# Kernel optimization log

Measured on AMD Instinct MI355X. Metric: run time of the kernel, lower is better.

## Reference

```python
import jax, jax.numpy as jnp
import numpy as np
from jax import lax

N = 50000        # num nodes
E = 800000       # edges per relation (no self loops; N self loops appended)
R = 3            # num_relations
F_IN = 256       # feature_size
C = 128          # hid_dim / channels
B = 4096         # batch_nodes
DT = 0.25
NSTEPS = 4       # n = ceil(time/dt) = ceil(1.0/0.25)


def setup_inputs() -> dict:
    key = jax.random.key(0)
    k1, k2, k3, k4, k5, k6, k7, k8 = jax.random.split(key, 8)
    features = jax.random.normal(k1, (N, F_IN), dtype=jnp.float32)
    # edges with no self loops: dst = (src + off) mod N, off in [1, N)
    src = jax.random.randint(k2, (R, E), 0, N)
    off = jax.random.randint(k3, (R, E), 1, N)
    dst = (src + off) % N
    edge_index = jnp.stack([src, dst], axis=1).astype(jnp.int64)  # [R, 2, E]
    batch_nodes = jax.random.randint(k4, (B,), 0, N).astype(jnp.int64)
    s = 1.0 / np.sqrt(F_IN)
    lin0_w = jax.random.normal(k5, (R, C, F_IN), dtype=jnp.float32) * s
    lin0_b = jax.random.normal(k6, (R, C), dtype=jnp.float32) * 0.01
    lin1_w = jax.random.normal(k7, (R, C, F_IN), dtype=jnp.float32) * s
    lin1_b = jax.random.normal(k8, (R, C), dtype=jnp.float32) * 0.01
    return {"features": features, "edge_index": edge_index, "batch_nodes": batch_nodes,
            "lin0_w": lin0_w, "lin0_b": lin0_b, "lin1_w": lin1_w, "lin1_b": lin1_b}


def _propagate(x, row, col, w):
    # out[i] = sum_{e: col[e]==i} w[e] * x[row[e]]   (gather-scale-scatter SpMM)
    return jax.ops.segment_sum(w[:, None] * x[row], col, num_segments=N)


def _wave_pde(x, row, col, w0, b0, w1, b1):
    # add_remaining_self_loops(fill=0.0): self loops appended at end with weight 0
    loops = jnp.arange(N, dtype=row.dtype)
    row_f = jnp.concatenate([row, loops])
    col_f = jnp.concatenate([col, loops])
    w_f = jnp.concatenate([jnp.ones((E,), x.dtype), jnp.zeros((N,), x.dtype)])
    # sym normalization: D^-1/2 A D^-1/2 (deg over col)
    deg = jax.ops.segment_sum(w_f, col_f, num_segments=N)
    dinv = jnp.where(deg > 0, lax.rsqrt(jnp.maximum(deg, 1e-30)), 0.0)
    w_norm = dinv[row_f] * w_f * dinv[col_f]
    # set_init_value
    phi0 = x @ w0.T + b0
    phi1 = x @ w1.T + b1
    # exp_conv_0 (exp_init=True): w' = dt^2*w/2; diag += 1; x1 = dt*phi1 + prop(phi0)
    w_init = (DT * DT * 0.5) * w_norm
    w_init = w_init.at[E:].add(1.0)
    x1 = DT * phi1 + _propagate(phi0, row_f, col_f, w_init)
    # time-stepping convs: w'' = dt^2*w; diag += 2; x_next = prop(x) - x_pre
    w_step = (DT * DT) * w_norm
    w_step = w_step.at[E:].add(2.0)

    def step(carry, _):
        xc, xp = carry
        xn = _propagate(xc, row_f, col_f, w_step) - xp
        return (xn, xc), None

    (x_out, _), _ = lax.scan(step, (x1, phi0), None, length=NSTEPS - 1)
    return x_out


def reference(features, edge_index, batch_nodes, lin0_w, lin0_b, lin1_w, lin1_b):
    # eval mode: dropout is identity
    embeds = []
    for r in range(R):
        row = edge_index[r, 0]
        col = edge_index[r, 1]
        x = _wave_pde(features, row, col, lin0_w[r], lin0_b[r], lin1_w[r], lin1_b[r])
        embeds.append(x[batch_nodes])  # [B, C]
    multi = jnp.stack(embeds, axis=1)  # [B, R, C]
    return multi.reshape(B, R * C)
```

## Files before the change

kernel.cpp:

```cpp
#include <hip/hip_runtime.h>
#include <hip/hip_bf16.h>

#define N_NODES 50000
#define N_EDGES 800000
#define N_REL   3
#define F_IN    256
#define CH      128
#define BATCH   4096
#define DT      0.25f
#define NRANGE  8
#define RSPAN   6250

typedef __bf16 bf16x8 __attribute__((ext_vector_type(8)));
typedef float f32x4 __attribute__((ext_vector_type(4)));

__device__ __forceinline__ ushort f2bf(float f) {
  unsigned u = __float_as_uint(f);
  return (ushort)((u + 0x7FFFu + ((u >> 16) & 1u)) >> 16);
}
__device__ __forceinline__ float bf2f(ushort h) {
  return __uint_as_float((unsigned)h << 16);
}

__global__ void k_detect(const int* __restrict__ ei, int* __restrict__ flag) {
  int lane = threadIdx.x;
  int v = ei[2 * lane + 1];
  unsigned long long m = __ballot(v != 0);
  if (lane == 0) flag[0] = (m == 0ull) ? 1 : 0;
}

__global__ void k_hist3x(const int* __restrict__ ei, const int* __restrict__ flag,
                         int* __restrict__ deg3) {
  int b = blockIdx.x;
  int q = b & (NRANGE - 1), chunk = b >> 3;
  int e = chunk * 256 + threadIdx.x;
  int r = blockIdx.y;
  if (e >= N_EDGES) return;
  long ci = (long)r * 2 * N_EDGES + N_EDGES + e;
  int d = flag[0] ? ei[2 * ci] : ei[ci];
  if (d / RSPAN == q) atomicAdd(&deg3[r * N_NODES + d], 1);
}

__global__ void k_dinv3(const int* __restrict__ deg3, float* __restrict__ dinv3,
                        int* __restrict__ flag) {
  int i = blockIdx.x * blockDim.x + threadIdx.x;
  if (i >= 3 * N_NODES) return;
  int d = deg3[i];
  if (d > 0) {
    dinv3[i] = rsqrtf((float)d);
  } else {
    dinv3[i] = 0.0f;
    atomicOr(&flag[1], 1);
  }
}

__global__ void k_scan3(const int* __restrict__ deg3, int* __restrict__ off3) {
  __shared__ int sm[1024];
  const int* deg = deg3 + blockIdx.x * N_NODES;
  int* off = off3 + blockIdx.x * (N_NODES + 1);
  int tid = threadIdx.x;
  const int PER = (N_NODES + 1023) / 1024;
  int base = tid * PER;
  int s = 0;
  for (int i = 0; i < PER; ++i) { int idx = base + i; if (idx < N_NODES) s += deg[idx]; }
  sm[tid] = s;
  __syncthreads();
  for (int d = 1; d < 1024; d <<= 1) {
    int v = 0;
    if (tid >= d) v = sm[tid - d];
    __syncthreads();
    sm[tid] += v;
    __syncthreads();
  }
  int run = sm[tid] - s;
  for (int i = 0; i < PER; ++i) {
    int idx = base + i;
    if (idx < N_NODES) { off[idx] = run; run += deg[idx]; }
  }
  if (tid == 1023) off[N_NODES] = run;
}

__global__ void k_fill3x(const int* __restrict__ ei, const int* __restrict__ flag,
                         const int* __restrict__ off3, int* __restrict__ cur3,
                         const float* __restrict__ dinv3, void* __restrict__ csrv) {
  int b = blockIdx.x;
  int q = b & (NRANGE - 1), chunk = b >> 3;
  int e = chunk * 256 + threadIdx.x;
  int r = blockIdx.y;
  if (e >= N_EDGES) return;
  int i64 = flag[0], iso = flag[1];
  long ri = (long)r * 2 * N_EDGES + e;
  long ci = ri + N_EDGES;
  int d = i64 ? ei[2 * ci] : ei[ci];
  if (d / RSPAN != q) return;
  int s = i64 ? ei[2 * ri] : ei[ri];
  int pos = atomicAdd(&cur3[r * N_NODES + d], 1);
  int slot = off3[r * (N_NODES + 1) + d] + pos;
  if (iso) {
    const float* dinv = dinv3 + r * N_NODES;
    ((int2*)csrv)[(size_t)r * N_EDGES + slot] =
        make_int2(s, __float_as_int(dinv[s] * dinv[d]));
  } else {
    ((int*)csrv)[(size_t)r * N_EDGES + slot] = s;
  }
}

__global__ __launch_bounds__(256) void k_phi_mfma(
    const float* __restrict__ X, const float* __restrict__ W0,
    const float* __restrict__ b0, const float* __restrict__ W1,
    const float* __restrict__ b1, const float* __restrict__ dinv,
    const int* __restrict__ flag, float* __restrict__ P0,
    float* __restrict__ P1) {
  __shared__ ushort Ah[128 * 32], Al[128 * 32], Bh[128 * 32], Bl[128 * 32];
  const int tid = threadIdx.x;
  const int m0 = blockIdx.x * 128;
  const float* W = blockIdx.y ? W1 : W0;
  const float* bias = blockIdx.y ? b1 : b0;
  float* P = blockIdx.y ? P1 : P0;
  const int wid = tid >> 6, lane = tid & 63;
  const int wr = wid >> 1, wc = wid & 1;
  const int lr = lane & 15, k8 = lane >> 4;
  const int rt = tid >> 1, kb = (tid & 1) * 16;
  const bool mok = (m0 + rt) < N_NODES;
  const float* Xrow = X + (size_t)(m0 + rt) * F_IN;
  const float* Wrow = W + (size_t)rt * F_IN;
  f32x4 acc[4][4] = {};
  for (int k0 = 0; k0 < F_IN; k0 += 32) {
    float4 xa[4], wb[4];
#pragma unroll
    for (int j = 0; j < 4; ++j) {
      xa[j] = mok ? *(const float4*)(Xrow + k0 + kb + 4 * j)
                  : make_float4(0.f, 0.f, 0.f, 0.f);
      wb[j] = *(const float4*)(Wrow + k0 + kb + 4 * j);
    }
    if (k0) __syncthreads();
#pragma unroll
    for (int j = 0; j < 4; ++j) {
      int idx = rt * 32 + kb + 4 * j;
      ushort h0 = f2bf(xa[j].x), h1 = f2bf(xa[j].y), h2 = f2bf(xa[j].z), h3 = f2bf(xa[j].w);
      *(ushort4*)&Ah[idx] = make_ushort4(h0, h1, h2, h3);
      *(ushort4*)&Al[idx] =
          make_ushort4(f2bf(xa[j].x - bf2f(h0)), f2bf(xa[j].y - bf2f(h1)),
                       f2bf(xa[j].z - bf2f(h2)), f2bf(xa[j].w - bf2f(h3)));
      ushort g0 = f2bf(wb[j].x), g1 = f2bf(wb[j].y), g2 = f2bf(wb[j].z), g3 = f2bf(wb[j].w);
      *(ushort4*)&Bh[idx] = make_ushort4(g0, g1, g2, g3);
      *(ushort4*)&Bl[idx] =
          make_ushort4(f2bf(wb[j].x - bf2f(g0)), f2bf(wb[j].y - bf2f(g1)),
                       f2bf(wb[j].z - bf2f(g2)), f2bf(wb[j].w - bf2f(g3)));
    }
    __syncthreads();
    bf16x8 ah[4], al[4], bh[4], bl[4];
#pragma unroll
    for (int i = 0; i < 4; ++i) {
      int ao = (wr * 64 + i * 16 + lr) * 32 + k8 * 8;
      int bo = (wc * 64 + i * 16 + lr) * 32 + k8 * 8;
      ah[i] = *(const bf16x8*)&Ah[ao];
      al[i] = *(const bf16x8*)&Al[ao];
      bh[i] = *(const bf16x8*)&Bh[bo];
      bl[i] = *(const bf16x8*)&Bl[bo];
    }
#pragma unroll
    for (int i = 0; i < 4; ++i)
#pragma unroll
      for (int j = 0; j < 4; ++j) {
        acc[i][j] = __builtin_amdgcn_mfma_f32_16x16x32_bf16(ah[i], bh[j], acc[i][j], 0, 0, 0);
        acc[i][j] = __builtin_amdgcn_mfma_f32_16x16x32_bf16(ah[i], bl[j], acc[i][j], 0, 0, 0);
        acc[i][j] = __builtin_amdgcn_mfma_f32_16x16x32_bf16(al[i], bh[j], acc[i][j], 0, 0, 0);
      }
  }
  int iso = flag[1];
  float rsc[4][4];
#pragma unroll
  for (int i = 0; i < 4; ++i)
#pragma unroll
    for (int q = 0; q < 4; ++q) {
      int m = m0 + wr * 64 + i * 16 + k8 * 4 + q;
      rsc[i][q] = (m < N_NODES && !iso) ? dinv[m] : 1.0f;
    }
#pragma unroll
  for (int j = 0; j < 4; ++j) {
    int ch = wc * 64 + j * 16 + lr;
    float bv = bias[ch];
#pragma unroll
    for (int i = 0; i < 4; ++i) {
      int mbase = m0 + wr * 64 + i * 16 + k8 * 4;
#pragma unroll
      for (int q = 0; q < 4; ++q) {
        int m = mbase + q;
        if (m < N_NODES) P[(size_t)m * CH + ch] = (acc[i][j][q] + bv) * rsc[i][q];
      }
    }
  }
}

__device__ __forceinline__ void prop_accum(
    const float* __restrict__ xc, const void* __restrict__ csrv, int r, int iso,
    int e0, int e1, int g, int l, float4& acc0, float4& acc1) {
  if (!iso) {
    const int* csr = (const int*)csrv + (size_t)r * N_EDGES;
    for (int e = e0; e < e1; e += 16) {
      int lim = e1 - 1;
      int src[4]; float wgt[4];
#pragma unroll
      for (int u = 0; u < 4; ++u) {
        int ee = e + 4 * u + g;
        src[u] = csr[min(ee, lim)];
        wgt[u] = (ee <= lim) ? 1.f : 0.f;
      }
      float4 va[4], vb[4];
#pragma unroll
      for (int u = 0; u < 4; ++u) {
        const float4* rs = (const float4*)(xc + (size_t)src[u] * CH);
        va[u] = rs[l];
        vb[u] = rs[l + 16];
      }
#pragma unroll
      for (int u = 0; u < 4; ++u) {
        float w0 = wgt[u];
        acc0.x = fmaf(w0, va[u].x, acc0.x); acc0.y = fmaf(w0, va[u].y, acc0.y);
        acc0.z = fmaf(w0, va[u].z, acc0.z); acc0.w = fmaf(w0, va[u].w, acc0.w);
        acc1.x = fmaf(w0, vb[u].x, acc1.x); acc1.y = fmaf(w0, vb[u].y, acc1.y);
        acc1.z = fmaf(w0, vb[u].z, acc1.z); acc1.w = fmaf(w0, vb[u].w, acc1.w);
      }
    }
  } else {
    const int2* csr = (const int2*)csrv + (size_t)r * N_EDGES;
    for (int e = e0; e < e1; e += 16) {
      int lim = e1 - 1;
      int2 pm[4]; float wgt[4];
#pragma unroll
      for (int u = 0; u < 4; ++u) {
        int ee = e + 4 * u + g;
        pm[u] = csr[min(ee, lim)];
        wgt[u] = (ee <= lim) ? __int_as_float(pm[u].y) : 0.f;
      }
      float4 va[4], vb[4];
#pragma unroll
      for (int u = 0; u < 4; ++u) {
        const float4* rs = (const float4*)(xc + (size_t)pm[u].x * CH);
        va[u] = rs[l];
        vb[u] = rs[l + 16];
      }
#pragma unroll
      for (int u = 0; u < 4; ++u) {
        float w0 = wgt[u];
        acc0.x = fmaf(w0, va[u].x, acc0.x); acc0.y = fmaf(w0, va[u].y, acc0.y);
        acc0.z = fmaf(w0, va[u].z, acc0.z); acc0.w = fmaf(w0, va[u].w, acc0.w);
        acc1.x = fmaf(w0, vb[u].x, acc1.x); acc1.y = fmaf(w0, vb[u].y, acc1.y);
        acc1.z = fmaf(w0, vb[u].z, acc1.z); acc1.w = fmaf(w0, vb[u].w, acc1.w);
      }
    }
  }
}

__global__ __launch_bounds__(256, 6) void k_prop(
    const float* __restrict__ xcb, const float* __restrict__ otherb,
    float* __restrict__ outb, const int* __restrict__ off3,
    const void* __restrict__ csrv, const int* __restrict__ flag, int rel0,
    size_t slab, float wscale, float aself, float beta) {
  int node = blockIdx.x * 4 + (threadIdx.x >> 6);
  if (node >= N_NODES) return;
  int rel = rel0 + blockIdx.y;
  const float* xc = xcb + (size_t)blockIdx.y * slab;
  const float* other = otherb + (size_t)blockIdx.y * slab;
  float* out = outb + (size_t)blockIdx.y * slab;
  const int* off = off3 + rel * (N_NODES + 1);
  int iso = flag[1];
  int lane = threadIdx.x & 63;
  int g = lane >> 4, l = lane & 15;
  int e0 = off[node], e1 = off[node + 1];
  size_t base = (size_t)node * CH;
  int go = (g & 1) * 64;
  float4 sv = *(const float4*)(xc + base + go + 4 * l);
  float4 ov = *(const float4*)(other + base + go + 4 * l);
  float4 acc0 = make_float4(0.f, 0.f, 0.f, 0.f);
  float4 acc1 = make_float4(0.f, 0.f, 0.f, 0.f);
  prop_accum(xc, csrv, rel, iso, e0, e1, g, l, acc0, acc1);
#pragma unroll
  for (int m = 16; m < 64; m <<= 1) {
    acc0.x += __shfl_xor(acc0.x, m); acc0.y += __shfl_xor(acc0.y, m);
    acc0.z += __shfl_xor(acc0.z, m); acc0.w += __shfl_xor(acc0.w, m);
    acc1.x += __shfl_xor(acc1.x, m); acc1.y += __shfl_xor(acc1.y, m);
    acc1.z += __shfl_xor(acc1.z, m); acc1.w += __shfl_xor(acc1.w, m);
  }
  float ws2 = iso ? wscale : ((e1 > e0) ? wscale / (float)(e1 - e0) : 0.f);
  if (g == 0) {
    float4 o;
    o.x = ws2 * acc0.x + aself * sv.x + beta * ov.x;
    o.y = ws2 * acc0.y + aself * sv.y + beta * ov.y;
    o.z = ws2 * acc0.z + aself * sv.z + beta * ov.z;
    o.w = ws2 * acc0.w + aself * sv.w + beta * ov.w;
    *(float4*)(out + base + 4 * l) = o;
  } else if (g == 1) {
    float4 o;
    o.x = ws2 * acc1.x + aself * sv.x + beta * ov.x;
    o.y = ws2 * acc1.y + aself * sv.y + beta * ov.y;
    o.z = ws2 * acc1.z + aself * sv.z + beta * ov.z;
    o.w = ws2 * acc1.w + aself * sv.w + beta * ov.w;
    *(float4*)(out + base + 64 + 4 * l) = o;
  }
}

__global__ __launch_bounds__(256) void k_gprop(
    const float* __restrict__ y3b, const float* __restrict__ y2b,
    const int* __restrict__ off3, const void* __restrict__ csrv,
    const int* __restrict__ flag, const int* __restrict__ batch,
    float* __restrict__ out, int rel0, size_t slab,
    float wscale, float aself, float beta) {
  int b = blockIdx.x * 4 + (threadIdx.x >> 6);
  if (b >= BATCH) return;
  int rel = rel0 + blockIdx.y;
  const float* y3 = y3b + (size_t)blockIdx.y * slab;
  const float* y2 = y2b + (size_t)blockIdx.y * slab;
  const int* off = off3 + rel * (N_NODES + 1);
  int i64 = flag[0], iso = flag[1];
  int node = i64 ? batch[2 * b] : batch[b];
  int lane = threadIdx.x & 63;
  int g = lane >> 4, l = lane & 15;
  int e0 = off[node], e1 = off[node + 1];
  size_t base = (size_t)node * CH;
  int go = (g & 1) * 64;
  float4 sv = *(const float4*)(y3 + base + go + 4 * l);
  float4 ov = *(const float4*)(y2 + base + go + 4 * l);
  float4 acc0 = make_float4(0.f, 0.f, 0.f, 0.f);
  float4 acc1 = make_float4(0.f, 0.f, 0.f, 0.f);
  prop_accum(y3, csrv, rel, iso, e0, e1, g, l, acc0, acc1);
#pragma unroll
  for (int m = 16; m < 64; m <<= 1) {
    acc0.x += __shfl_xor(acc0.x, m); acc0.y += __shfl_xor(acc0.y, m);
    acc0.z += __shfl_xor(acc0.z, m); acc0.w += __shfl_xor(acc0.w, m);
    acc1.x += __shfl_xor(acc1.x, m); acc1.y += __shfl_xor(acc1.y, m);
    acc1.z += __shfl_xor(acc1.z, m); acc1.w += __shfl_xor(acc1.w, m);
  }
  int deg = e1 - e0;
  float ws2 = iso ? wscale : ((deg > 0) ? wscale / (float)deg : 0.f);
  float osc = iso ? 1.0f : sqrtf((float)deg);
  float* orow = out + (size_t)b * (N_REL * CH) + rel * CH;
  if (g == 0) {
    float4 o;
    o.x = osc * (ws2 * acc0.x + aself * sv.x + beta * ov.x);
    o.y = osc * (ws2 * acc0.y + aself * sv.y + beta * ov.y);
    o.z = osc * (ws2 * acc0.z + aself * sv.z + beta * ov.z);
    o.w = osc * (ws2 * acc0.w + aself * sv.w + beta * ov.w);
    *(float4*)(orow + 4 * l) = o;
  } else if (g == 1) {
    float4 o;
    o.x = osc * (ws2 * acc1.x + aself * sv.x + beta * ov.x);
    o.y = osc * (ws2 * acc1.y + aself * sv.y + beta * ov.y);
    o.z = osc * (ws2 * acc1.z + aself * sv.z + beta * ov.z);
    o.w = osc * (ws2 * acc1.w + aself * sv.w + beta * ov.w);
    *(float4*)(orow + 64 + 4 * l) = o;
  }
}

extern "C" void kernel_launch(void* const* d_in, const int* in_sizes, int n_in,
                              void* d_out, int out_size, void* d_ws, size_t ws_size,
                              hipStream_t stream) {
  const float* features   = (const float*)d_in[0];
  const int*   edge_index = (const int*)d_in[1];
  const int*   batch_nodes= (const int*)d_in[2];
  const float* lin0_w     = (const float*)d_in[3];
  const float* lin0_b     = (const float*)d_in[4];
  const float* lin1_w     = (const float*)d_in[5];
  const float* lin1_b     = (const float*)d_in[6];
  float* out = (float*)d_out;

  const size_t slabElems = (size_t)N_NODES * CH;
  const size_t fixedBytes = 256 + 4 * (((size_t)3 * N_NODES * 4 + 255) & ~(size_t)255)
                            + (((size_t)3 * N_EDGES * 8 + 255) & ~(size_t)255) + 4096;
  const size_t fusedNeed = fixedBytes + 2 * 3 * slabElems * 4;
  const bool fused = ws_size >= fusedNeed;
  const size_t slab = fused ? slabElems : 0;
  const int nslab = fused ? 3 : 1;

  char* w = (char*)d_ws;
  size_t o = 0;
  auto nxt = [&](size_t bytes) {
    char* p = w + o;
    o = (o + bytes + 255) & ~(size_t)255;
    return p;
  };
  int*   flag  = (int*)  nxt(256);
  int*   deg3  = (int*)  nxt((size_t)3 * N_NODES * 4);
  int*   cur3  = (int*)  nxt((size_t)3 * N_NODES * 4);
  float* dinv3 = (float*)nxt((size_t)3 * N_NODES * 4);
  int*   off3  = (int*)  nxt((size_t)3 * (N_NODES + 1) * 4);
  void*  csr   = (void*) nxt((size_t)3 * N_EDGES * 8);
  float* A     = (float*)nxt((size_t)nslab * slabElems * 4);
  float* B     = (float*)nxt((size_t)nslab * slabElems * 4);

  hipMemsetAsync(flag, 0, 8, stream);
  hipMemsetAsync(deg3, 0, (size_t)3 * N_NODES * 4, stream);
  hipMemsetAsync(cur3, 0, (size_t)3 * N_NODES * 4, stream);
  k_detect<<<1, 64, 0, stream>>>(edge_index, flag);
  const int NCHUNK = (N_EDGES + 255) / 256;
  k_hist3x<<<dim3(NCHUNK * NRANGE, 3), 256, 0, stream>>>(edge_index, flag, deg3);
  k_dinv3<<<(3 * N_NODES + 255) / 256, 256, 0, stream>>>(deg3, dinv3, flag);
  k_scan3<<<3, 1024, 0, stream>>>(deg3, off3);
  k_fill3x<<<dim3(NCHUNK * NRANGE, 3), 256, 0, stream>>>(edge_index, flag, off3,
                                                         cur3, dinv3, csr);

  const float h2 = DT * DT;
  for (int r = 0; r < N_REL; ++r) {
    float* Ar = A + (size_t)(fused ? r : 0) * slabElems;
    float* Br = B + (size_t)(fused ? r : 0) * slabElems;
    if (!fused && r > 0) break;
    k_phi_mfma<<<dim3((N_NODES + 127) / 128, 2), 256, 0, stream>>>(
        features, lin0_w + (size_t)r * CH * F_IN, lin0_b + (size_t)r * CH,
        lin1_w + (size_t)r * CH * F_IN, lin1_b + (size_t)r * CH,
        dinv3 + r * N_NODES, flag, Ar, Br);
  }

  if (fused) {
    k_prop<<<dim3((N_NODES + 3) / 4, 3), 256, 0, stream>>>(
        A, B, B, off3, csr, flag, 0, slab, 0.5f * h2, 1.0f, DT);
    k_prop<<<dim3((N_NODES + 3) / 4, 3), 256, 0, stream>>>(
        B, A, A, off3, csr, flag, 0, slab, h2, 2.0f, -1.0f);
    k_prop<<<dim3((N_NODES + 3) / 4, 3), 256, 0, stream>>>(
        A, B, B, off3, csr, flag, 0, slab, h2, 2.0f, -1.0f);
    k_gprop<<<dim3((BATCH + 3) / 4, 3), 256, 0, stream>>>(
        B, A, off3, csr, flag, batch_nodes, out, 0, slab, h2, 2.0f, -1.0f);
  } else {
    for (int r = 0; r < N_REL; ++r) {
      if (r > 0) {
        k_phi_mfma<<<dim3((N_NODES + 127) / 128, 2), 256, 0, stream>>>(
            features, lin0_w + (size_t)r * CH * F_IN, lin0_b + (size_t)r * CH,
            lin1_w + (size_t)r * CH * F_IN, lin1_b + (size_t)r * CH,
            dinv3 + r * N_NODES, flag, A, B);
      }
      k_prop<<<dim3((N_NODES + 3) / 4, 1), 256, 0, stream>>>(
          A, B, B, off3, csr, flag, r, 0, 0.5f * h2, 1.0f, DT);
      k_prop<<<dim3((N_NODES + 3) / 4, 1), 256, 0, stream>>>(
          B, A, A, off3, csr, flag, r, 0, h2, 2.0f, -1.0f);
      k_prop<<<dim3((N_NODES + 3) / 4, 1), 256, 0, stream>>>(
          A, B, B, off3, csr, flag, r, 0, h2, 2.0f, -1.0f);
      k_gprop<<<dim3((BATCH + 3) / 4, 1), 256, 0, stream>>>(
          B, A, off3, csr, flag, batch_nodes, out, r, 0, h2, 2.0f, -1.0f);
    }
  }
}
```

Before: 1.136 ms.

## Gather neighbor features from a bf16 mirror in fused propagation steps

```diff
diff --git a/kernel.cpp b/kernel.cpp
--- a/kernel.cpp
+++ b/kernel.cpp
@@ -193,6 +193,124 @@
   }
 }
 
+__global__ void k_mir(const float* __restrict__ src, ushort* __restrict__ dst,
+                      long n8) {
+  long i = (long)blockIdx.x * 256 + threadIdx.x;
+  if (i >= n8) return;
+  f32x4 a = *(const f32x4*)(src + i * 8);
+  f32x4 b = *(const f32x4*)(src + i * 8 + 4);
+  uint4 m;
+  m.x = (unsigned)f2bf(a[0]) | ((unsigned)f2bf(a[1]) << 16);
+  m.y = (unsigned)f2bf(a[2]) | ((unsigned)f2bf(a[3]) << 16);
+  m.z = (unsigned)f2bf(b[0]) | ((unsigned)f2bf(b[1]) << 16);
+  m.w = (unsigned)f2bf(b[2]) | ((unsigned)f2bf(b[3]) << 16);
+  *(uint4*)(dst + i * 8) = m;
+}
+
+__device__ __forceinline__ void bf8_fma(uint4 v, float w, f32x4& a0, f32x4& a1) {
+  a0[0] = fmaf(w, __uint_as_float(v.x << 16), a0[0]);
+  a0[1] = fmaf(w, __uint_as_float(v.x & 0xffff0000u), a0[1]);
+  a0[2] = fmaf(w, __uint_as_float(v.y << 16), a0[2]);
+  a0[3] = fmaf(w, __uint_as_float(v.y & 0xffff0000u), a0[3]);
+  a1[0] = fmaf(w, __uint_as_float(v.z << 16), a1[0]);
+  a1[1] = fmaf(w, __uint_as_float(v.z & 0xffff0000u), a1[1]);
+  a1[2] = fmaf(w, __uint_as_float(v.w << 16), a1[2]);
+  a1[3] = fmaf(w, __uint_as_float(v.w & 0xffff0000u), a1[3]);
+}
+
+__global__ __launch_bounds__(256, 8) void k_prop_m(
+    const float* __restrict__ xcb, const ushort* __restrict__ mirb,
+    const float* __restrict__ otherb, float* __restrict__ outb,
+    ushort* __restrict__ omirb, const int* __restrict__ off3,
+    const void* __restrict__ csrv, const int* __restrict__ flag,
+    size_t slab, float wscale, float aself, float beta) {
+  int node = blockIdx.x * 4 + (threadIdx.x >> 6);
+  if (node >= N_NODES) return;
+  int rel = blockIdx.y;
+  const float*  xc    = xcb   + (size_t)rel * slab;
+  const ushort* mir   = mirb  + (size_t)rel * slab;
+  const float*  other = otherb+ (size_t)rel * slab;
+  float*        out   = outb  + (size_t)rel * slab;
+  ushort*       omir  = omirb + (size_t)rel * slab;
+  const int* off = off3 + rel * (N_NODES + 1);
+  int iso = flag[1];
+  int lane = threadIdx.x & 63;
+  int g = lane >> 4, l = lane & 15;
+  int e0 = off[node], e1 = off[node + 1];
+  size_t base = (size_t)node * CH;
+  int co = l * 8;
+  f32x4 sv0 = {}, sv1 = {}, ov0 = {}, ov1 = {};
+  if (g == 0) {
+    sv0 = __builtin_nontemporal_load((const f32x4*)(xc + base + co));
+    sv1 = __builtin_nontemporal_load((const f32x4*)(xc + base + co + 4));
+    ov0 = __builtin_nontemporal_load((const f32x4*)(other + base + co));
+    ov1 = __builtin_nontemporal_load((const f32x4*)(other + base + co + 4));
+  }
+  f32x4 a0 = {}, a1 = {};
+  if (!iso) {
+    const int* csr = (const int*)csrv + (size_t)rel * N_EDGES;
+    for (int e = e0; e < e1; e += 16) {
+      int lim = e1 - 1;
+      int src[4]; float wgt[4];
+#pragma unroll
+      for (int u = 0; u < 4; ++u) {
+        int ee = e + 4 * u + g;
+        src[u] = csr[min(ee, lim)];
+        wgt[u] = (ee <= lim) ? 1.f : 0.f;
+      }
+      uint4 v[4];
+#pragma unroll
+      for (int u = 0; u < 4; ++u)
+        v[u] = *(const uint4*)(mir + (size_t)src[u] * CH + co);
+#pragma unroll
+      for (int u = 0; u < 4; ++u) bf8_fma(v[u], wgt[u], a0, a1);
+    }
+  } else {
+    const int2* csr = (const int2*)csrv + (size_t)rel * N_EDGES;
+    for (int e = e0; e < e1; e += 16) {
+      int lim = e1 - 1;
+      int2 pm[4]; float wgt[4];
+#pragma unroll
+      for (int u = 0; u < 4; ++u) {
+        int ee = e + 4 * u + g;
+        pm[u] = csr[min(ee, lim)];
+        wgt[u] = (ee <= lim) ? __int_as_float(pm[u].y) : 0.f;
+      }
+      uint4 v[4];
+#pragma unroll
+      for (int u = 0; u < 4; ++u)
+        v[u] = *(const uint4*)(mir + (size_t)pm[u].x * CH + co);
+#pragma unroll
+      for (int u = 0; u < 4; ++u) bf8_fma(v[u], wgt[u], a0, a1);
+    }
+  }
+#pragma unroll
+  for (int m = 16; m < 64; m <<= 1) {
+#pragma unroll
+    for (int i = 0; i < 4; ++i) {
+      a0[i] += __shfl_xor(a0[i], m);
+      a1[i] += __shfl_xor(a1[i], m);
+    }
+  }
+  if (g == 0) {
+    float ws2 = iso ? wscale : ((e1 > e0) ? wscale / (float)(e1 - e0) : 0.f);
+    f32x4 o0, o1;
+#pragma unroll
+    for (int i = 0; i < 4; ++i) {
+      o0[i] = ws2 * a0[i] + aself * sv0[i] + beta * ov0[i];
+      o1[i] = ws2 * a1[i] + aself * sv1[i] + beta * ov1[i];
+    }
+    __builtin_nontemporal_store(o0, (f32x4*)(out + base + co));
+    __builtin_nontemporal_store(o1, (f32x4*)(out + base + co + 4));
+    uint4 m;
+    m.x = (unsigned)f2bf(o0[0]) | ((unsigned)f2bf(o0[1]) << 16);
+    m.y = (unsigned)f2bf(o0[2]) | ((unsigned)f2bf(o0[3]) << 16);
+    m.z = (unsigned)f2bf(o1[0]) | ((unsigned)f2bf(o1[1]) << 16);
+    m.w = (unsigned)f2bf(o1[2]) | ((unsigned)f2bf(o1[3]) << 16);
+    *(uint4*)(omir + base + co) = m;
+  }
+}
+
 __device__ __forceinline__ void prop_accum(
     const float* __restrict__ xc, const void* __restrict__ csrv, int r, int iso,
     int e0, int e1, int g, int l, float4& acc0, float4& acc1) {
@@ -253,7 +371,7 @@
   }
 }
 
-__global__ __launch_bounds__(256, 6) void k_prop(
+__global__ __launch_bounds__(256, 8) void k_prop(
     const float* __restrict__ xcb, const float* __restrict__ otherb,
     float* __restrict__ outb, const int* __restrict__ off3,
     const void* __restrict__ csrv, const int* __restrict__ flag, int rel0,
@@ -366,12 +484,6 @@
   float* out = (float*)d_out;
 
   const size_t slabElems = (size_t)N_NODES * CH;
-  const size_t fixedBytes = 256 + 4 * (((size_t)3 * N_NODES * 4 + 255) & ~(size_t)255)
-                            + (((size_t)3 * N_EDGES * 8 + 255) & ~(size_t)255) + 4096;
-  const size_t fusedNeed = fixedBytes + 2 * 3 * slabElems * 4;
-  const bool fused = ws_size >= fusedNeed;
-  const size_t slab = fused ? slabElems : 0;
-  const int nslab = fused ? 3 : 1;
 
   char* w = (char*)d_ws;
   size_t o = 0;
@@ -386,8 +498,14 @@
   float* dinv3 = (float*)nxt((size_t)3 * N_NODES * 4);
   int*   off3  = (int*)  nxt((size_t)3 * (N_NODES + 1) * 4);
   void*  csr   = (void*) nxt((size_t)3 * N_EDGES * 8);
-  float* A     = (float*)nxt((size_t)nslab * slabElems * 4);
-  float* B     = (float*)nxt((size_t)nslab * slabElems * 4);
+  size_t avail = (ws_size > o) ? ws_size - o : 0;
+  const bool fused = avail >= 2 * 3 * slabElems * 4 + 4096;
+  const bool mirOk = avail >= 2 * 3 * slabElems * 4 + 2 * 3 * slabElems * 2 + 8192;
+  const int nslab = fused ? 3 : 1;
+  float*  A    = (float*) nxt((size_t)nslab * slabElems * 4);
+  float*  B    = (float*) nxt((size_t)nslab * slabElems * 4);
+  ushort* Amir = mirOk ? (ushort*)nxt((size_t)3 * slabElems * 2) : nullptr;
+  ushort* Bmir = mirOk ? (ushort*)nxt((size_t)3 * slabElems * 2) : nullptr;
 
   hipMemsetAsync(flag, 0, 8, stream);
   hipMemsetAsync(deg3, 0, (size_t)3 * N_NODES * 4, stream);
@@ -401,33 +519,39 @@
                                                          cur3, dinv3, csr);
 
   const float h2 = DT * DT;
-  for (int r = 0; r < N_REL; ++r) {
-    float* Ar = A + (size_t)(fused ? r : 0) * slabElems;
-    float* Br = B + (size_t)(fused ? r : 0) * slabElems;
-    if (!fused && r > 0) break;
-    k_phi_mfma<<<dim3((N_NODES + 127) / 128, 2), 256, 0, stream>>>(
-        features, lin0_w + (size_t)r * CH * F_IN, lin0_b + (size_t)r * CH,
-        lin1_w + (size_t)r * CH * F_IN, lin1_b + (size_t)r * CH,
-        dinv3 + r * N_NODES, flag, Ar, Br);
-  }
-
   if (fused) {
-    k_prop<<<dim3((N_NODES + 3) / 4, 3), 256, 0, stream>>>(
-        A, B, B, off3, csr, flag, 0, slab, 0.5f * h2, 1.0f, DT);
-    k_prop<<<dim3((N_NODES + 3) / 4, 3), 256, 0, stream>>>(
-        B, A, A, off3, csr, flag, 0, slab, h2, 2.0f, -1.0f);
-    k_prop<<<dim3((N_NODES + 3) / 4, 3), 256, 0, stream>>>(
-        A, B, B, off3, csr, flag, 0, slab, h2, 2.0f, -1.0f);
+    for (int r = 0; r < N_REL; ++r) {
+      k_phi_mfma<<<dim3((N_NODES + 127) / 128, 2), 256, 0, stream>>>(
+          features, lin0_w + (size_t)r * CH * F_IN, lin0_b + (size_t)r * CH,
+          lin1_w + (size_t)r * CH * F_IN, lin1_b + (size_t)r * CH,
+          dinv3 + r * N_NODES, flag, A + (size_t)r * slabElems,
+          B + (size_t)r * slabElems);
+    }
+    const long n8 = (long)3 * slabElems / 8;
+    if (mirOk) {
+      k_mir<<<(int)((n8 + 255) / 256), 256, 0, stream>>>(A, Amir, n8);
+      k_prop_m<<<dim3((N_NODES + 3) / 4, 3), 256, 0, stream>>>(
+          A, Amir, B, B, Bmir, off3, csr, flag, slabElems, 0.5f * h2, 1.0f, DT);
+      k_prop_m<<<dim3((N_NODES + 3) / 4, 3), 256, 0, stream>>>(
+          B, Bmir, A, A, Amir, off3, csr, flag, slabElems, h2, 2.0f, -1.0f);
+      k_prop_m<<<dim3((N_NODES + 3) / 4, 3), 256, 0, stream>>>(
+          A, Amir, B, B, Bmir, off3, csr, flag, slabElems, h2, 2.0f, -1.0f);
+    } else {
+      k_prop<<<dim3((N_NODES + 3) / 4, 3), 256, 0, stream>>>(
+          A, B, B, off3, csr, flag, 0, slabElems, 0.5f * h2, 1.0f, DT);
+      k_prop<<<dim3((N_NODES + 3) / 4, 3), 256, 0, stream>>>(
+          B, A, A, off3, csr, flag, 0, slabElems, h2, 2.0f, -1.0f);
+      k_prop<<<dim3((N_NODES + 3) / 4, 3), 256, 0, stream>>>(
+          A, B, B, off3, csr, flag, 0, slabElems, h2, 2.0f, -1.0f);
+    }
     k_gprop<<<dim3((BATCH + 3) / 4, 3), 256, 0, stream>>>(
-        B, A, off3, csr, flag, batch_nodes, out, 0, slab, h2, 2.0f, -1.0f);
+        B, A, off3, csr, flag, batch_nodes, out, 0, slabElems, h2, 2.0f, -1.0f);
   } else {
     for (int r = 0; r < N_REL; ++r) {
-      if (r > 0) {
-        k_phi_mfma<<<dim3((N_NODES + 127) / 128, 2), 256, 0, stream>>>(
-            features, lin0_w + (size_t)r * CH * F_IN, lin0_b + (size_t)r * CH,
-            lin1_w + (size_t)r * CH * F_IN, lin1_b + (size_t)r * CH,
-            dinv3 + r * N_NODES, flag, A, B);
-      }
+      k_phi_mfma<<<dim3((N_NODES + 127) / 128, 2), 256, 0, stream>>>(
+          features, lin0_w + (size_t)r * CH * F_IN, lin0_b + (size_t)r * CH,
+          lin1_w + (size_t)r * CH * F_IN, lin1_b + (size_t)r * CH,
+          dinv3 + r * N_NODES, flag, A, B);
       k_prop<<<dim3((N_NODES + 3) / 4, 1), 256, 0, stream>>>(
           A, B, B, off3, csr, flag, r, 0, 0.5f * h2, 1.0f, DT);
       k_prop<<<dim3((N_NODES + 3) / 4, 1), 256, 0, stream>>>(
```

New measurement: 1.151 ms. No clear change (+1.4%).
